# Kernel tuning notes

Measured on AMD Instinct MI355X. Metric: run time of the kernel, lower is better.

## Reference

```python
import jax, jax.numpy as jnp
from jax import lax
import numpy as np

GROUPS = 32  # EMA 'factor'
EPS = 1e-5   # torch GroupNorm default eps


def setup_inputs() -> dict:
    key = jax.random.key(0)
    ks = jax.random.split(key, 3)
    B, C, H, W = 8, 256, 128, 128
    cg = C // GROUPS  # channels per group = 8
    x = jax.random.normal(ks[0], (B, C, H, W), dtype=jnp.float32)
    w1 = jax.random.normal(ks[1], (cg, cg), dtype=jnp.float32) * 0.1    # conv1x1 weight (O,I)
    b1 = jnp.zeros((cg,), dtype=jnp.float32)
    w3 = jax.random.normal(ks[2], (cg, cg, 3, 3), dtype=jnp.float32) * 0.1  # conv3x3 weight (O,I,kh,kw)
    b3 = jnp.zeros((cg,), dtype=jnp.float32)
    gn_w = jnp.ones((cg,), dtype=jnp.float32)
    gn_b = jnp.zeros((cg,), dtype=jnp.float32)
    return {"x": x, "w1": w1, "b1": b1, "w3": w3, "b3": b3, "gn_w": gn_w, "gn_b": gn_b}


def reference(x, w1, b1, w3, b3, gn_w, gn_b):
    b, c, h, w = x.shape
    g = GROUPS
    cg = c // g
    gx = x.reshape(b * g, cg, h, w)                       # [bg, cg, h, w]
    # directional pooling (AdaptiveAvgPool over one axis)
    x_h = gx.mean(axis=3, keepdims=True)                  # [bg, cg, h, 1]
    x_w = gx.mean(axis=2, keepdims=True).transpose(0, 1, 3, 2)  # [bg, cg, w, 1]
    hw = jnp.concatenate([x_h, x_w], axis=2)              # [bg, cg, h+w, 1]
    hw = jnp.einsum('oi,bilk->bolk', w1, hw) + b1[None, :, None, None]
    xh = hw[:, :, :h]                                      # [bg, cg, h, 1]
    xw = hw[:, :, h:].transpose(0, 1, 3, 2)                # [bg, cg, 1, w]
    gated = gx * jax.nn.sigmoid(xh) * jax.nn.sigmoid(xw)
    # GroupNorm(cg groups over cg channels) == per-channel norm over (h, w)
    mu = gated.mean(axis=(2, 3), keepdims=True)
    var = gated.var(axis=(2, 3), keepdims=True)
    x1 = (gated - mu) / jnp.sqrt(var + EPS) * gn_w[None, :, None, None] + gn_b[None, :, None, None]
    # 3x3 conv branch
    x2 = lax.conv_general_dilated(gx, w3, (1, 1), 'SAME',
                                  dimension_numbers=('NCHW', 'OIHW', 'NCHW'))
    x2 = x2 + b3[None, :, None, None]
    # cross-branch channel-attention matmuls
    x11 = jax.nn.softmax(x1.mean(axis=(2, 3)), axis=-1)[:, None, :]  # [bg, 1, cg]
    x21 = jax.nn.softmax(x2.mean(axis=(2, 3)), axis=-1)[:, None, :]  # [bg, 1, cg]
    x12 = x2.reshape(b * g, cg, h * w)
    x22 = x1.reshape(b * g, cg, h * w)
    weights = (jnp.matmul(x11, x12) + jnp.matmul(x21, x22)).reshape(b * g, 1, h, w)
    return (gx * jax.nn.sigmoid(weights)).reshape(b, c, h, w)
```

## Files before the change

kernel.cpp:

```cpp
#include <hip/hip_runtime.h>
#include <cstdint>

#define EPS 1e-5f


__global__ __launch_bounds__(256) void passA(const float* __restrict__ x,
                                             float* __restrict__ rowsum,
                                             float* __restrict__ colsum) {
    int p = blockIdx.x;
    int t = threadIdx.x;
    const float4* xp = (const float4*)(x + (size_t)p * 16384);
    float4 csum = {0.f, 0.f, 0.f, 0.f};
    for (int i = 0; i < 16; ++i) {
        float4 v = xp[i * 256 + t];
        csum.x += v.x; csum.y += v.y; csum.z += v.z; csum.w += v.w;
        float rs = v.x + v.y + v.z + v.w;
        for (int m = 16; m; m >>= 1) rs += __shfl_xor(rs, m);
        if ((t & 31) == 0) rowsum[p * 128 + i * 8 + (t >> 5)] = rs;
    }
    __shared__ float4 red[256];
    red[t] = csum;
    __syncthreads();
    if (t < 32) {
        float4 s = red[t];
        for (int j = 1; j < 8; ++j) {
            float4 v = red[j * 32 + t];
            s.x += v.x; s.y += v.y; s.z += v.z; s.w += v.w;
        }
        ((float4*)colsum)[p * 32 + t] = s;
    }
}

__global__ __launch_bounds__(128) void passB(const float* __restrict__ x,
                                             const float* __restrict__ rowsum,
                                             const float* __restrict__ colsum,
                                             const float* __restrict__ w1,
                                             const float* __restrict__ b1,
                                             const float* __restrict__ w3,
                                             const float* __restrict__ b3,
                                             const float* __restrict__ gn_b,
                                             float* __restrict__ sh,
                                             float* __restrict__ sw,
                                             float* __restrict__ x21,
                                             float* __restrict__ wt) {
    int bg = blockIdx.x;
    int t = threadIdx.x;
    __shared__ float rs[8][128], cs[8][128];
    __shared__ float S[8], Tm[72], corners[8][4], m2[8];
    __shared__ float w1l[64], b1l[8], x11l[8];

    for (int i = 0; i < 8; ++i) {
        rs[i][t] = rowsum[(bg * 8 + i) * 128 + t];
        cs[i][t] = colsum[(bg * 8 + i) * 128 + t];
    }
    if (t < 64) w1l[t] = w1[t];
    if (t < 8) b1l[t] = b1[t];
    if (t < 8) {
        const float* xp = x + (size_t)(bg * 8 + t) * 16384;
        corners[t][0] = xp[0];
        corners[t][1] = xp[127];
        corners[t][2] = xp[127 * 128];
        corners[t][3] = xp[127 * 128 + 127];
    }
    __syncthreads();

    if (t < 8) {
        float s = 0.f;
        for (int y = 0; y < 128; ++y) s += rs[t][y];
        S[t] = s;
    }
    {
        const float inv128 = 1.f / 128.f;
        int y = t;
        for (int o = 0; o < 8; ++o) {
            float ar = b1l[o], ac = b1l[o];
            for (int i = 0; i < 8; ++i) {
                ar += w1l[o * 8 + i] * rs[i][y] * inv128;
                ac += w1l[o * 8 + i] * cs[i][y] * inv128;
            }
            sh[(bg * 8 + o) * 128 + y] = 1.f / (1.f + __expf(-ar));
            sw[(bg * 8 + o) * 128 + y] = 1.f / (1.f + __expf(-ac));
        }
    }
    __syncthreads();

    if (t < 72) {
        int i = t / 9, ky = (t % 9) / 3, kx = t % 3;
        float v = S[i];
        if (ky == 0) v -= rs[i][127]; else if (ky == 2) v -= rs[i][0];
        if (kx == 0) v -= cs[i][127]; else if (kx == 2) v -= cs[i][0];
        if (ky == 0 && kx == 0) v += corners[i][3];
        if (ky == 0 && kx == 2) v += corners[i][2];
        if (ky == 2 && kx == 0) v += corners[i][1];
        if (ky == 2 && kx == 2) v += corners[i][0];
        Tm[t] = v;
    }
    __syncthreads();

    if (t < 8) {
        float acc = 0.f;
        for (int j = 0; j < 72; ++j) acc += w3[t * 72 + j] * Tm[j];
        m2[t] = b3[t] + acc * (1.f / 16384.f);
    }
    __syncthreads();

    if (t == 0) {
        float mx = m2[0];
        for (int i = 1; i < 8; ++i) mx = fmaxf(mx, m2[i]);
        float e[8], s = 0.f;
        for (int i = 0; i < 8; ++i) { e[i] = __expf(m2[i] - mx); s += e[i]; }
        for (int i = 0; i < 8; ++i) x21[bg * 8 + i] = e[i] / s;
    }

    if (bg == 0) {
        if (t == 0) {
            float mx = gn_b[0];
            for (int i = 1; i < 8; ++i) mx = fmaxf(mx, gn_b[i]);
            float e[8], s = 0.f;
            for (int i = 0; i < 8; ++i) { e[i] = __expf(gn_b[i] - mx); s += e[i]; }
            for (int i = 0; i < 8; ++i) x11l[i] = e[i] / s;
        }
        __syncthreads();
        if (t < 72) {
            float a = 0.f;
            for (int o = 0; o < 8; ++o) a += x11l[o] * w3[o * 72 + t];
            wt[t] = a;
        }
        if (t == 72) {
            float a = 0.f;
            for (int o = 0; o < 8; ++o) a += x11l[o] * b3[o];
            wt[72] = a;
        }
    }
}

__global__ __launch_bounds__(256) void passC(const float* __restrict__ x,
                                             const float* __restrict__ sh,
                                             const float* __restrict__ sw,
                                             float* __restrict__ musum,
                                             float* __restrict__ sqsum) {
    int p = blockIdx.x;
    int t = threadIdx.x;
    __shared__ float shl[128];
    __shared__ float4 swl[32];
    if (t < 128) shl[t] = sh[p * 128 + t];
    if (t < 32) swl[t] = ((const float4*)sw)[p * 32 + t];
    __syncthreads();
    const float4* xp = (const float4*)(x + (size_t)p * 16384);
    float4 sw4 = swl[t & 31];
    float s = 0.f, q = 0.f;
    for (int i = 0; i < 16; ++i) {
        float4 v = xp[i * 256 + t];
        float shv = shl[i * 8 + (t >> 5)];
        float g0 = v.x * shv * sw4.x;
        float g1 = v.y * shv * sw4.y;
        float g2 = v.z * shv * sw4.z;
        float g3 = v.w * shv * sw4.w;
        s += g0 + g1 + g2 + g3;
        q += g0 * g0 + g1 * g1 + g2 * g2 + g3 * g3;
    }
    for (int m = 32; m; m >>= 1) { s += __shfl_xor(s, m); q += __shfl_xor(q, m); }
    __shared__ float rsum[4], rsq[4];
    if ((t & 63) == 0) { rsum[t >> 6] = s; rsq[t >> 6] = q; }
    __syncthreads();
    if (t == 0) {
        musum[p] = rsum[0] + rsum[1] + rsum[2] + rsum[3];
        sqsum[p] = rsq[0] + rsq[1] + rsq[2] + rsq[3];
    }
}

__global__ __launch_bounds__(64) void passD(const float* __restrict__ musum,
                                            const float* __restrict__ sqsum,
                                            const float* __restrict__ x21,
                                            const float* __restrict__ gn_w,
                                            const float* __restrict__ gn_b,
                                            const float* __restrict__ wt,
                                            float* __restrict__ alpha,
                                            float* __restrict__ beta) {
    int bg = blockIdx.x;
    int t = threadIdx.x;
    __shared__ float bs[8];
    if (t < 8) {
        int p = bg * 8 + t;
        float mu = musum[p] * (1.f / 16384.f);
        float ex2 = sqsum[p] * (1.f / 16384.f);
        float var = ex2 - mu * mu;
        float inv = rsqrtf(var + EPS);
        float a = x21[p] * inv * gn_w[t];
        alpha[p] = a;
        bs[t] = x21[p] * (gn_b[t] - mu * inv * gn_w[t]);
    }
    __syncthreads();
    if (t == 0) {
        float s = wt[72];
        for (int i = 0; i < 8; ++i) s += bs[i];
        beta[bg] = s;
    }
}

__global__ __launch_bounds__(256) void passE(const float* __restrict__ x,
                                             const float* __restrict__ sh,
                                             const float* __restrict__ sw,
                                             const float* __restrict__ alpha,
                                             const float* __restrict__ beta,
                                             const float* __restrict__ wt,
                                             float* __restrict__ out) {
    int blk = blockIdx.x;
    int bg = blk >> 4;
    int r0 = (blk & 15) * 8;
    int t = threadIdx.x;
    __shared__ float tl[8 * 10 * 132];
    __shared__ float swl[8 * 128];
    __shared__ float ashl[64];
    __shared__ float wtl[73];
    __shared__ float betal;
    const size_t pbase = (size_t)(bg * 8) * 16384;

    for (int it = 0; it < 10; ++it) {
        int idx = it * 256 + t;
        int i = idx / 320, rem = idx % 320;
        int rr = rem / 32, c4 = rem % 32;
        int g = r0 - 1 + rr;
        float4 v = {0.f, 0.f, 0.f, 0.f};
        if (g >= 0 && g < 128)
            v = *(const float4*)(x + pbase + (size_t)i * 16384 + g * 128 + c4 * 4);
        float* d = &tl[(i * 10 + rr) * 132 + 1 + c4 * 4];
        d[0] = v.x; d[1] = v.y; d[2] = v.z; d[3] = v.w;
        if (c4 == 0) d[-1] = 0.f;
        if (c4 == 31) d[4] = 0.f;
    }
    {
        ((float4*)swl)[t] = ((const float4*)sw)[(size_t)(bg * 8 + (t >> 5)) * 32 + (t & 31)];
    }
    if (t < 64) {
        int i = t >> 3, y = t & 7;
        ashl[t] = alpha[bg * 8 + i] * sh[(bg * 8 + i) * 128 + r0 + y];
    }
    if (t < 73) wtl[t] = wt[t];
    if (t == 255) betal = beta[bg];
    __syncthreads();

    int y = t >> 5;
    int x0 = (t & 31) * 4;
    float acc0, acc1, acc2, acc3;
    acc0 = acc1 = acc2 = acc3 = betal;
    float gv[8][4];
#pragma unroll
    for (int i = 0; i < 8; ++i) {
        const float* base = &tl[(i * 10 + y) * 132 + x0];
#pragma unroll
        for (int ky = 0; ky < 3; ++ky) {
            float4 va = *(const float4*)(base + ky * 132);
            float4 vb = *(const float4*)(base + ky * 132 + 4);
            float w0 = wtl[i * 9 + ky * 3 + 0];
            float w1 = wtl[i * 9 + ky * 3 + 1];
            float w2 = wtl[i * 9 + ky * 3 + 2];
            acc0 += w0 * va.x + w1 * va.y + w2 * va.z;
            acc1 += w0 * va.y + w1 * va.z + w2 * va.w;
            acc2 += w0 * va.z + w1 * va.w + w2 * vb.x;
            acc3 += w0 * va.w + w1 * vb.x + w2 * vb.y;
            if (ky == 1) { gv[i][0] = va.y; gv[i][1] = va.z; gv[i][2] = va.w; gv[i][3] = vb.x; }
        }
        float as = ashl[i * 8 + y];
        float s0 = swl[i * 128 + x0 + 0];
        float s1 = swl[i * 128 + x0 + 1];
        float s2 = swl[i * 128 + x0 + 2];
        float s3 = swl[i * 128 + x0 + 3];
        acc0 += as * s0 * gv[i][0];
        acc1 += as * s1 * gv[i][1];
        acc2 += as * s2 * gv[i][2];
        acc3 += as * s3 * gv[i][3];
    }
    float sg0 = 1.f / (1.f + __expf(-acc0));
    float sg1 = 1.f / (1.f + __expf(-acc1));
    float sg2 = 1.f / (1.f + __expf(-acc2));
    float sg3 = 1.f / (1.f + __expf(-acc3));
    size_t ob = pbase + (size_t)(r0 + y) * 128 + x0;
#pragma unroll
    for (int c = 0; c < 8; ++c) {
        float4 o4 = { gv[c][0] * sg0, gv[c][1] * sg1, gv[c][2] * sg2, gv[c][3] * sg3 };
        *(float4*)(out + ob + (size_t)c * 16384) = o4;
    }
}

extern "C" void kernel_launch(void* const* d_in, const int* in_sizes, int n_in,
                              void* d_out, int out_size, void* d_ws, size_t ws_size,
                              hipStream_t stream) {
    (void)in_sizes; (void)n_in; (void)out_size; (void)ws_size;
    const float* x    = (const float*)d_in[0];
    const float* w1   = (const float*)d_in[1];
    const float* b1   = (const float*)d_in[2];
    const float* w3   = (const float*)d_in[3];
    const float* b3   = (const float*)d_in[4];
    const float* gn_w = (const float*)d_in[5];
    const float* gn_b = (const float*)d_in[6];
    float* out = (float*)d_out;
    float* ws  = (float*)d_ws;

    float* rowsum = ws;
    float* colsum = ws + 262144;
    float* sh     = ws + 524288;
    float* sw     = ws + 786432;
    float* x21    = ws + 1048576;
    float* musum  = ws + 1050624;
    float* sqsum  = ws + 1052672;
    float* alpha  = ws + 1054720;
    float* beta   = ws + 1056768;
    float* wt     = ws + 1057024;

    hipLaunchKernelGGL(passA, dim3(2048), dim3(256), 0, stream, x, rowsum, colsum);
    hipLaunchKernelGGL(passB, dim3(256),  dim3(128), 0, stream, x, rowsum, colsum,
                       w1, b1, w3, b3, gn_b, sh, sw, x21, wt);
    hipLaunchKernelGGL(passC, dim3(2048), dim3(256), 0, stream, x, sh, sw, musum, sqsum);
    hipLaunchKernelGGL(passD, dim3(256),  dim3(64),  0, stream, musum, sqsum, x21,
                       gn_w, gn_b, wt, alpha, beta);
    hipLaunchKernelGGL(passE, dim3(4096), dim3(256), 0, stream, x, sh, sw,
                       alpha, beta, wt, out);
}
```

Measured before the change: 118.0 us.

## Fuse all five passes into one persistent kernel per group

Replaces the five separate kernels with a single kernel that runs one 1024-thread block per batch-group. Row and column sums, the pooling gates, the GroupNorm statistics, the softmax weights and the final conv-gated output are all computed in that block, with intermediates kept in LDS. This drops the workspace round trips and four kernel launches. In exchange, each CU runs one large block through serialized phases separated by barriers, which may hide memory latency less well. The block also needs about 150KB of LDS.

```diff
diff --git a/kernel.cpp b/kernel.cpp
--- a/kernel.cpp
+++ b/kernel.cpp
@@ -3,290 +3,258 @@
 
 #define EPS 1e-5f
 
-
-__global__ __launch_bounds__(256) void passA(const float* __restrict__ x,
-                                             float* __restrict__ rowsum,
-                                             float* __restrict__ colsum) {
-    int p = blockIdx.x;
-    int t = threadIdx.x;
-    const float4* xp = (const float4*)(x + (size_t)p * 16384);
-    float4 csum = {0.f, 0.f, 0.f, 0.f};
-    for (int i = 0; i < 16; ++i) {
-        float4 v = xp[i * 256 + t];
-        csum.x += v.x; csum.y += v.y; csum.z += v.z; csum.w += v.w;
-        float rs = v.x + v.y + v.z + v.w;
-        for (int m = 16; m; m >>= 1) rs += __shfl_xor(rs, m);
-        if ((t & 31) == 0) rowsum[p * 128 + i * 8 + (t >> 5)] = rs;
-    }
-    __shared__ float4 red[256];
-    red[t] = csum;
-    __syncthreads();
-    if (t < 32) {
-        float4 s = red[t];
-        for (int j = 1; j < 8; ++j) {
-            float4 v = red[j * 32 + t];
-            s.x += v.x; s.y += v.y; s.z += v.z; s.w += v.w;
-        }
-        ((float4*)colsum)[p * 32 + t] = s;
-    }
-}
-
-__global__ __launch_bounds__(128) void passB(const float* __restrict__ x,
-                                             const float* __restrict__ rowsum,
-                                             const float* __restrict__ colsum,
-                                             const float* __restrict__ w1,
-                                             const float* __restrict__ b1,
-                                             const float* __restrict__ w3,
-                                             const float* __restrict__ b3,
-                                             const float* __restrict__ gn_b,
-                                             float* __restrict__ sh,
-                                             float* __restrict__ sw,
-                                             float* __restrict__ x21,
-                                             float* __restrict__ wt) {
-    int bg = blockIdx.x;
-    int t = threadIdx.x;
-    __shared__ float rs[8][128], cs[8][128];
-    __shared__ float S[8], Tm[72], corners[8][4], m2[8];
-    __shared__ float w1l[64], b1l[8], x11l[8];
-
-    for (int i = 0; i < 8; ++i) {
-        rs[i][t] = rowsum[(bg * 8 + i) * 128 + t];
-        cs[i][t] = colsum[(bg * 8 + i) * 128 + t];
-    }
-    if (t < 64) w1l[t] = w1[t];
-    if (t < 8) b1l[t] = b1[t];
-    if (t < 8) {
-        const float* xp = x + (size_t)(bg * 8 + t) * 16384;
-        corners[t][0] = xp[0];
-        corners[t][1] = xp[127];
-        corners[t][2] = xp[127 * 128];
-        corners[t][3] = xp[127 * 128 + 127];
-    }
-    __syncthreads();
-
+#define LDS_TL    0
+#define LDS_SH    35904
+#define LDS_SW    36928
+#define LDS_S     37952
+#define LDS_TM    37960
+#define LDS_CORN  38032
+#define LDS_M2    38064
+#define LDS_X11   38072
+#define LDS_X21   38080
+#define LDS_W1L   38088
+#define LDS_B1L   38152
+#define LDS_WTL   38160
+#define LDS_PS    38240
+#define LDS_QS    38304
+#define LDS_AL    38368
+#define LDS_BS    38376
+#define LDS_BETA  38384
+#define LDS_TOTAL 38400
+
+__global__ __launch_bounds__(1024) void fused_adaptatt(
+    const float* __restrict__ x,
+    const float* __restrict__ w1, const float* __restrict__ b1,
+    const float* __restrict__ w3, const float* __restrict__ b3,
+    const float* __restrict__ gn_w, const float* __restrict__ gn_b,
+    float* __restrict__ out)
+{
+    extern __shared__ float lds[];
+    const int bg = blockIdx.x;
+    const int t  = threadIdx.x;
+    const int sg = t >> 8;
+    const int ts = t & 255;
+    float* rs = lds;
+    float* cs = lds + 1024;
+    float4* red = (float4*)(lds + 2048);
+    const size_t pbase = (size_t)(bg * 8) * 16384;
+
+    for (int half = 0; half < 2; ++half) {
+        int pi = half * 4 + sg;
+        const float4* xp = (const float4*)(x + pbase + (size_t)pi * 16384);
+        float4 csum = {0.f, 0.f, 0.f, 0.f};
+        for (int i = 0; i < 16; ++i) {
+            float4 v = xp[i * 256 + ts];
+            csum.x += v.x; csum.y += v.y; csum.z += v.z; csum.w += v.w;
+            float rsv = v.x + v.y + v.z + v.w;
+            for (int m = 16; m; m >>= 1) rsv += __shfl_xor(rsv, m);
+            if ((ts & 31) == 0) rs[pi * 128 + i * 8 + (ts >> 5)] = rsv;
+        }
+        red[sg * 256 + ts] = csum;
+        __syncthreads();
+        if (ts < 32) {
+            float4 s = red[sg * 256 + ts];
+            for (int j = 1; j < 8; ++j) {
+                float4 v = red[sg * 256 + j * 32 + ts];
+                s.x += v.x; s.y += v.y; s.z += v.z; s.w += v.w;
+            }
+            ((float4*)(cs + pi * 128))[ts] = s;
+        }
+        __syncthreads();
+    }
+
+    if (t < 64) lds[LDS_W1L + t] = w1[t];
+    if (t >= 64 && t < 72) lds[LDS_B1L + (t - 64)] = b1[t - 64];
+    if (t >= 128 && t < 136) {
+        int i = t - 128;
+        const float* xpp = x + pbase + (size_t)i * 16384;
+        lds[LDS_CORN + i * 4 + 0] = xpp[0];
+        lds[LDS_CORN + i * 4 + 1] = xpp[127];
+        lds[LDS_CORN + i * 4 + 2] = xpp[127 * 128];
+        lds[LDS_CORN + i * 4 + 3] = xpp[127 * 128 + 127];
+    }
+    if (t == 200) {
+        float mx = gn_b[0];
+        for (int i = 1; i < 8; ++i) mx = fmaxf(mx, gn_b[i]);
+        float e[8], s = 0.f;
+        for (int i = 0; i < 8; ++i) { e[i] = __expf(gn_b[i] - mx); s += e[i]; }
+        for (int i = 0; i < 8; ++i) lds[LDS_X11 + i] = e[i] / s;
+    }
+    __syncthreads();
+
+    {
+        int o = t >> 7, y = t & 127;
+        const float inv128 = 1.f / 128.f;
+        float ar = lds[LDS_B1L + o], ac = ar;
+        for (int i = 0; i < 8; ++i) {
+            float w = lds[LDS_W1L + o * 8 + i];
+            ar += w * rs[i * 128 + y] * inv128;
+            ac += w * cs[i * 128 + y] * inv128;
+        }
+        lds[LDS_SH + o * 128 + y] = 1.f / (1.f + __expf(-ar));
+        lds[LDS_SW + o * 128 + y] = 1.f / (1.f + __expf(-ac));
+    }
     if (t < 8) {
         float s = 0.f;
-        for (int y = 0; y < 128; ++y) s += rs[t][y];
-        S[t] = s;
-    }
-    {
-        const float inv128 = 1.f / 128.f;
-        int y = t;
-        for (int o = 0; o < 8; ++o) {
-            float ar = b1l[o], ac = b1l[o];
-            for (int i = 0; i < 8; ++i) {
-                ar += w1l[o * 8 + i] * rs[i][y] * inv128;
-                ac += w1l[o * 8 + i] * cs[i][y] * inv128;
-            }
-            sh[(bg * 8 + o) * 128 + y] = 1.f / (1.f + __expf(-ar));
-            sw[(bg * 8 + o) * 128 + y] = 1.f / (1.f + __expf(-ac));
-        }
+        for (int y = 0; y < 128; ++y) s += rs[t * 128 + y];
+        lds[LDS_S + t] = s;
     }
     __syncthreads();
 
     if (t < 72) {
         int i = t / 9, ky = (t % 9) / 3, kx = t % 3;
-        float v = S[i];
-        if (ky == 0) v -= rs[i][127]; else if (ky == 2) v -= rs[i][0];
-        if (kx == 0) v -= cs[i][127]; else if (kx == 2) v -= cs[i][0];
-        if (ky == 0 && kx == 0) v += corners[i][3];
-        if (ky == 0 && kx == 2) v += corners[i][2];
-        if (ky == 2 && kx == 0) v += corners[i][1];
-        if (ky == 2 && kx == 2) v += corners[i][0];
-        Tm[t] = v;
+        float v = lds[LDS_S + i];
+        if (ky == 0) v -= rs[i * 128 + 127]; else if (ky == 2) v -= rs[i * 128 + 0];
+        if (kx == 0) v -= cs[i * 128 + 127]; else if (kx == 2) v -= cs[i * 128 + 0];
+        if (ky == 0 && kx == 0) v += lds[LDS_CORN + i * 4 + 3];
+        if (ky == 0 && kx == 2) v += lds[LDS_CORN + i * 4 + 2];
+        if (ky == 2 && kx == 0) v += lds[LDS_CORN + i * 4 + 1];
+        if (ky == 2 && kx == 2) v += lds[LDS_CORN + i * 4 + 0];
+        lds[LDS_TM + t] = v;
     }
     __syncthreads();
 
     if (t < 8) {
         float acc = 0.f;
-        for (int j = 0; j < 72; ++j) acc += w3[t * 72 + j] * Tm[j];
-        m2[t] = b3[t] + acc * (1.f / 16384.f);
+        for (int j = 0; j < 72; ++j) acc += w3[t * 72 + j] * lds[LDS_TM + j];
+        lds[LDS_M2 + t] = b3[t] + acc * (1.f / 16384.f);
+    }
+    if (t >= 128 && t < 201) {
+        int j = t - 128;
+        float a = 0.f;
+        if (j < 72) { for (int o = 0; o < 8; ++o) a += lds[LDS_X11 + o] * w3[o * 72 + j]; }
+        else        { for (int o = 0; o < 8; ++o) a += lds[LDS_X11 + o] * b3[o]; }
+        lds[LDS_WTL + j] = a;
     }
     __syncthreads();
 
     if (t == 0) {
-        float mx = m2[0];
-        for (int i = 1; i < 8; ++i) mx = fmaxf(mx, m2[i]);
+        float mx = lds[LDS_M2];
+        for (int i = 1; i < 8; ++i) mx = fmaxf(mx, lds[LDS_M2 + i]);
         float e[8], s = 0.f;
-        for (int i = 0; i < 8; ++i) { e[i] = __expf(m2[i] - mx); s += e[i]; }
-        for (int i = 0; i < 8; ++i) x21[bg * 8 + i] = e[i] / s;
-    }
-
-    if (bg == 0) {
-        if (t == 0) {
-            float mx = gn_b[0];
-            for (int i = 1; i < 8; ++i) mx = fmaxf(mx, gn_b[i]);
-            float e[8], s = 0.f;
-            for (int i = 0; i < 8; ++i) { e[i] = __expf(gn_b[i] - mx); s += e[i]; }
-            for (int i = 0; i < 8; ++i) x11l[i] = e[i] / s;
-        }
-        __syncthreads();
-        if (t < 72) {
-            float a = 0.f;
-            for (int o = 0; o < 8; ++o) a += x11l[o] * w3[o * 72 + t];
-            wt[t] = a;
-        }
-        if (t == 72) {
-            float a = 0.f;
-            for (int o = 0; o < 8; ++o) a += x11l[o] * b3[o];
-            wt[72] = a;
-        }
-    }
-}
-
-__global__ __launch_bounds__(256) void passC(const float* __restrict__ x,
-                                             const float* __restrict__ sh,
-                                             const float* __restrict__ sw,
-                                             float* __restrict__ musum,
-                                             float* __restrict__ sqsum) {
-    int p = blockIdx.x;
-    int t = threadIdx.x;
-    __shared__ float shl[128];
-    __shared__ float4 swl[32];
-    if (t < 128) shl[t] = sh[p * 128 + t];
-    if (t < 32) swl[t] = ((const float4*)sw)[p * 32 + t];
-    __syncthreads();
-    const float4* xp = (const float4*)(x + (size_t)p * 16384);
-    float4 sw4 = swl[t & 31];
-    float s = 0.f, q = 0.f;
-    for (int i = 0; i < 16; ++i) {
-        float4 v = xp[i * 256 + t];
-        float shv = shl[i * 8 + (t >> 5)];
-        float g0 = v.x * shv * sw4.x;
-        float g1 = v.y * shv * sw4.y;
-        float g2 = v.z * shv * sw4.z;
-        float g3 = v.w * shv * sw4.w;
-        s += g0 + g1 + g2 + g3;
-        q += g0 * g0 + g1 * g1 + g2 * g2 + g3 * g3;
-    }
-    for (int m = 32; m; m >>= 1) { s += __shfl_xor(s, m); q += __shfl_xor(q, m); }
-    __shared__ float rsum[4], rsq[4];
-    if ((t & 63) == 0) { rsum[t >> 6] = s; rsq[t >> 6] = q; }
-    __syncthreads();
-    if (t == 0) {
-        musum[p] = rsum[0] + rsum[1] + rsum[2] + rsum[3];
-        sqsum[p] = rsq[0] + rsq[1] + rsq[2] + rsq[3];
-    }
-}
-
-__global__ __launch_bounds__(64) void passD(const float* __restrict__ musum,
-                                            const float* __restrict__ sqsum,
-                                            const float* __restrict__ x21,
-                                            const float* __restrict__ gn_w,
-                                            const float* __restrict__ gn_b,
-                                            const float* __restrict__ wt,
-                                            float* __restrict__ alpha,
-                                            float* __restrict__ beta) {
-    int bg = blockIdx.x;
-    int t = threadIdx.x;
-    __shared__ float bs[8];
+        for (int i = 0; i < 8; ++i) { e[i] = __expf(lds[LDS_M2 + i] - mx); s += e[i]; }
+        for (int i = 0; i < 8; ++i) lds[LDS_X21 + i] = e[i] / s;
+    }
+    __syncthreads();
+
+    float* shl = lds + LDS_SH;
+    float* swl = lds + LDS_SW;
+    for (int half = 0; half < 2; ++half) {
+        int pi = half * 4 + sg;
+        const float4* xp = (const float4*)(x + pbase + (size_t)pi * 16384);
+        float4 sw4 = ((const float4*)(swl + pi * 128))[ts & 31];
+        float s = 0.f, q = 0.f;
+        for (int i = 0; i < 16; ++i) {
+            float4 v = xp[i * 256 + ts];
+            float shv = shl[pi * 128 + i * 8 + (ts >> 5)];
+            float g0 = v.x * shv * sw4.x;
+            float g1 = v.y * shv * sw4.y;
+            float g2 = v.z * shv * sw4.z;
+            float g3 = v.w * shv * sw4.w;
+            s += g0 + g1 + g2 + g3;
+            q += g0 * g0 + g1 * g1 + g2 * g2 + g3 * g3;
+        }
+        for (int m = 16; m; m >>= 1) { s += __shfl_xor(s, m); q += __shfl_xor(q, m); }
+        if ((ts & 31) == 0) {
+            lds[LDS_PS + pi * 8 + (ts >> 5)] = s;
+            lds[LDS_QS + pi * 8 + (ts >> 5)] = q;
+        }
+    }
+    __syncthreads();
     if (t < 8) {
-        int p = bg * 8 + t;
-        float mu = musum[p] * (1.f / 16384.f);
-        float ex2 = sqsum[p] * (1.f / 16384.f);
+        float s = 0.f, q = 0.f;
+        for (int j = 0; j < 8; ++j) { s += lds[LDS_PS + t * 8 + j]; q += lds[LDS_QS + t * 8 + j]; }
+        float mu  = s * (1.f / 16384.f);
+        float ex2 = q * (1.f / 16384.f);
         float var = ex2 - mu * mu;
         float inv = rsqrtf(var + EPS);
-        float a = x21[p] * inv * gn_w[t];
-        alpha[p] = a;
-        bs[t] = x21[p] * (gn_b[t] - mu * inv * gn_w[t]);
+        float x21v = lds[LDS_X21 + t];
+        lds[LDS_AL + t] = x21v * inv * gn_w[t];
+        lds[LDS_BS + t] = x21v * (gn_b[t] - mu * inv * gn_w[t]);
     }
     __syncthreads();
     if (t == 0) {
-        float s = wt[72];
-        for (int i = 0; i < 8; ++i) s += bs[i];
-        beta[bg] = s;
-    }
-}
-
-__global__ __launch_bounds__(256) void passE(const float* __restrict__ x,
-                                             const float* __restrict__ sh,
-                                             const float* __restrict__ sw,
-                                             const float* __restrict__ alpha,
-                                             const float* __restrict__ beta,
-                                             const float* __restrict__ wt,
-                                             float* __restrict__ out) {
-    int blk = blockIdx.x;
-    int bg = blk >> 4;
-    int r0 = (blk & 15) * 8;
-    int t = threadIdx.x;
-    __shared__ float tl[8 * 10 * 132];
-    __shared__ float swl[8 * 128];
-    __shared__ float ashl[64];
-    __shared__ float wtl[73];
-    __shared__ float betal;
-    const size_t pbase = (size_t)(bg * 8) * 16384;
-
-    for (int it = 0; it < 10; ++it) {
-        int idx = it * 256 + t;
-        int i = idx / 320, rem = idx % 320;
-        int rr = rem / 32, c4 = rem % 32;
-        int g = r0 - 1 + rr;
-        float4 v = {0.f, 0.f, 0.f, 0.f};
-        if (g >= 0 && g < 128)
-            v = *(const float4*)(x + pbase + (size_t)i * 16384 + g * 128 + c4 * 4);
-        float* d = &tl[(i * 10 + rr) * 132 + 1 + c4 * 4];
-        d[0] = v.x; d[1] = v.y; d[2] = v.z; d[3] = v.w;
-        if (c4 == 0) d[-1] = 0.f;
-        if (c4 == 31) d[4] = 0.f;
-    }
-    {
-        ((float4*)swl)[t] = ((const float4*)sw)[(size_t)(bg * 8 + (t >> 5)) * 32 + (t & 31)];
-    }
-    if (t < 64) {
-        int i = t >> 3, y = t & 7;
-        ashl[t] = alpha[bg * 8 + i] * sh[(bg * 8 + i) * 128 + r0 + y];
-    }
-    if (t < 73) wtl[t] = wt[t];
-    if (t == 255) betal = beta[bg];
-    __syncthreads();
-
-    int y = t >> 5;
-    int x0 = (t & 31) * 4;
-    float acc0, acc1, acc2, acc3;
-    acc0 = acc1 = acc2 = acc3 = betal;
-    float gv[8][4];
-#pragma unroll
-    for (int i = 0; i < 8; ++i) {
-        const float* base = &tl[(i * 10 + y) * 132 + x0];
-#pragma unroll
-        for (int ky = 0; ky < 3; ++ky) {
-            float4 va = *(const float4*)(base + ky * 132);
-            float4 vb = *(const float4*)(base + ky * 132 + 4);
-            float w0 = wtl[i * 9 + ky * 3 + 0];
-            float w1 = wtl[i * 9 + ky * 3 + 1];
-            float w2 = wtl[i * 9 + ky * 3 + 2];
-            acc0 += w0 * va.x + w1 * va.y + w2 * va.z;
-            acc1 += w0 * va.y + w1 * va.z + w2 * va.w;
-            acc2 += w0 * va.z + w1 * va.w + w2 * vb.x;
-            acc3 += w0 * va.w + w1 * vb.x + w2 * vb.y;
-            if (ky == 1) { gv[i][0] = va.y; gv[i][1] = va.z; gv[i][2] = va.w; gv[i][3] = vb.x; }
-        }
-        float as = ashl[i * 8 + y];
-        float s0 = swl[i * 128 + x0 + 0];
-        float s1 = swl[i * 128 + x0 + 1];
-        float s2 = swl[i * 128 + x0 + 2];
-        float s3 = swl[i * 128 + x0 + 3];
-        acc0 += as * s0 * gv[i][0];
-        acc1 += as * s1 * gv[i][1];
-        acc2 += as * s2 * gv[i][2];
-        acc3 += as * s3 * gv[i][3];
-    }
-    float sg0 = 1.f / (1.f + __expf(-acc0));
-    float sg1 = 1.f / (1.f + __expf(-acc1));
-    float sg2 = 1.f / (1.f + __expf(-acc2));
-    float sg3 = 1.f / (1.f + __expf(-acc3));
-    size_t ob = pbase + (size_t)(r0 + y) * 128 + x0;
-#pragma unroll
-    for (int c = 0; c < 8; ++c) {
-        float4 o4 = { gv[c][0] * sg0, gv[c][1] * sg1, gv[c][2] * sg2, gv[c][3] * sg3 };
-        *(float4*)(out + ob + (size_t)c * 16384) = o4;
+        float s = lds[LDS_WTL + 72];
+        for (int i = 0; i < 8; ++i) s += lds[LDS_BS + i];
+        lds[LDS_BETA] = s;
+    }
+    __syncthreads();
+
+    const float beta_v = lds[LDS_BETA];
+    for (int ch = 0; ch < 4; ++ch) {
+        int r0 = ch * 32;
+        __syncthreads();
+        {
+            int rr = t >> 5, c4 = t & 31;
+            int g = r0 - 1 + rr;
+#pragma unroll
+            for (int i = 0; i < 8; ++i) {
+                float4 v = {0.f, 0.f, 0.f, 0.f};
+                if (g >= 0 && g < 128)
+                    v = *(const float4*)(x + pbase + (size_t)i * 16384 + g * 128 + c4 * 4);
+                float* d = &lds[(i * 34 + rr) * 132 + 1 + c4 * 4];
+                d[0] = v.x; d[1] = v.y; d[2] = v.z; d[3] = v.w;
+                if (c4 == 0)  d[-1] = 0.f;
+                if (c4 == 31) d[4]  = 0.f;
+                if (t < 64) {
+                    int rr2 = 32 + rr;
+                    int g2 = r0 - 1 + rr2;
+                    float4 v2 = {0.f, 0.f, 0.f, 0.f};
+                    if (g2 < 128)
+                        v2 = *(const float4*)(x + pbase + (size_t)i * 16384 + g2 * 128 + c4 * 4);
+                    float* d2 = &lds[(i * 34 + rr2) * 132 + 1 + c4 * 4];
+                    d2[0] = v2.x; d2[1] = v2.y; d2[2] = v2.z; d2[3] = v2.w;
+                    if (c4 == 0)  d2[-1] = 0.f;
+                    if (c4 == 31) d2[4]  = 0.f;
+                }
+            }
+        }
+        __syncthreads();
+        int y = t >> 5;
+        int x0 = (t & 31) * 4;
+        float acc0, acc1, acc2, acc3;
+        acc0 = acc1 = acc2 = acc3 = beta_v;
+        float gv[8][4];
+#pragma unroll
+        for (int i = 0; i < 8; ++i) {
+            const float* base = &lds[(i * 34 + y) * 132 + x0];
+#pragma unroll
+            for (int ky = 0; ky < 3; ++ky) {
+                float4 va = *(const float4*)(base + ky * 132);
+                float4 vb = *(const float4*)(base + ky * 132 + 4);
+                float w0 = lds[LDS_WTL + i * 9 + ky * 3 + 0];
+                float w1v = lds[LDS_WTL + i * 9 + ky * 3 + 1];
+                float w2 = lds[LDS_WTL + i * 9 + ky * 3 + 2];
+                acc0 += w0 * va.x + w1v * va.y + w2 * va.z;
+                acc1 += w0 * va.y + w1v * va.z + w2 * va.w;
+                acc2 += w0 * va.z + w1v * va.w + w2 * vb.x;
+                acc3 += w0 * va.w + w1v * vb.x + w2 * vb.y;
+                if (ky == 1) { gv[i][0] = va.y; gv[i][1] = va.z; gv[i][2] = va.w; gv[i][3] = vb.x; }
+            }
+            float as = lds[LDS_AL + i] * shl[i * 128 + r0 + y];
+            float4 s4 = *(const float4*)(swl + i * 128 + x0);
+            acc0 += as * s4.x * gv[i][0];
+            acc1 += as * s4.y * gv[i][1];
+            acc2 += as * s4.z * gv[i][2];
+            acc3 += as * s4.w * gv[i][3];
+        }
+        float sg0 = 1.f / (1.f + __expf(-acc0));
+        float sg1 = 1.f / (1.f + __expf(-acc1));
+        float sg2 = 1.f / (1.f + __expf(-acc2));
+        float sg3 = 1.f / (1.f + __expf(-acc3));
+        size_t ob = pbase + (size_t)(r0 + y) * 128 + x0;
+#pragma unroll
+        for (int c = 0; c < 8; ++c) {
+            float4 o4 = { gv[c][0] * sg0, gv[c][1] * sg1, gv[c][2] * sg2, gv[c][3] * sg3 };
+            *(float4*)(out + ob + (size_t)c * 16384) = o4;
+        }
     }
 }
 
 extern "C" void kernel_launch(void* const* d_in, const int* in_sizes, int n_in,
                               void* d_out, int out_size, void* d_ws, size_t ws_size,
                               hipStream_t stream) {
-    (void)in_sizes; (void)n_in; (void)out_size; (void)ws_size;
+    (void)in_sizes; (void)n_in; (void)out_size; (void)d_ws; (void)ws_size;
     const float* x    = (const float*)d_in[0];
     const float* w1   = (const float*)d_in[1];
     const float* b1   = (const float*)d_in[2];
@@ -295,25 +263,7 @@
     const float* gn_w = (const float*)d_in[5];
     const float* gn_b = (const float*)d_in[6];
     float* out = (float*)d_out;
-    float* ws  = (float*)d_ws;
-
-    float* rowsum = ws;
-    float* colsum = ws + 262144;
-    float* sh     = ws + 524288;
-    float* sw     = ws + 786432;
-    float* x21    = ws + 1048576;
-    float* musum  = ws + 1050624;
-    float* sqsum  = ws + 1052672;
-    float* alpha  = ws + 1054720;
-    float* beta   = ws + 1056768;
-    float* wt     = ws + 1057024;
-
-    hipLaunchKernelGGL(passA, dim3(2048), dim3(256), 0, stream, x, rowsum, colsum);
-    hipLaunchKernelGGL(passB, dim3(256),  dim3(128), 0, stream, x, rowsum, colsum,
-                       w1, b1, w3, b3, gn_b, sh, sw, x21, wt);
-    hipLaunchKernelGGL(passC, dim3(2048), dim3(256), 0, stream, x, sh, sw, musum, sqsum);
-    hipLaunchKernelGGL(passD, dim3(256),  dim3(64),  0, stream, musum, sqsum, x21,
-                       gn_w, gn_b, wt, alpha, beta);
-    hipLaunchKernelGGL(passE, dim3(4096), dim3(256), 0, stream, x, sh, sw,
-                       alpha, beta, wt, out);
+
+    hipLaunchKernelGGL(fused_adaptatt, dim3(256), dim3(1024), LDS_TOTAL * 4, stream,
+                       x, w1, b1, w3, b3, gn_w, gn_b, out);
 }
```

After: 118.5 us. About the same (+0.4%).
